# Kernel tuning notes

Hardware: AMD Instinct MI355X
Metric: run time of the kernel (lower is better)

## Reference

```python
import math
import jax, jax.numpy as jnp
import numpy as np

B, T, C = 2, 2048, 2048
H, G = 16, 4          # n_head, n_group
HKV = H // G          # kv heads
HD = C // H           # head dim = 128

def setup_inputs() -> dict:
    key = jax.random.key(0)
    ks = jax.random.split(key, 4)
    s = 0.02  # realistic init scale
    return {
        "x": jax.random.normal(ks[0], (B, T, C), jnp.float32),
        "Wkv": jax.random.normal(ks[1], (C, 2 * C // G), jnp.float32) * s,
        "bkv": jnp.zeros((2 * C // G,), jnp.float32),
        "Wq": jax.random.normal(ks[2], (C, C), jnp.float32) * s,
        "bq": jnp.zeros((C,), jnp.float32),
        "Wp": jax.random.normal(ks[3], (C, C), jnp.float32) * s,
        "bp": jnp.zeros((C,), jnp.float32),
    }

def _expand_kv(t):
    # (B,T,HKV*HD) -> replicate each kv head G times -> (B,H,T,HD)
    t = t.reshape(B, T, HKV, HD)
    t = jnp.broadcast_to(t[:, :, None], (B, T, G, HKV, HD)).reshape(B, T, H, HD)
    return t.transpose(0, 2, 1, 3)

def reference(x, Wkv, bkv, Wq, bq, Wp, bp):
    kv = x @ Wkv + bkv                      # (B,T,2C/G)
    k, v = jnp.split(kv, 2, axis=-1)
    q = (x @ Wq + bq).reshape(B, T, H, HD).transpose(0, 2, 1, 3)  # (B,H,T,HD)
    k = _expand_kv(k)
    v = _expand_kv(v)
    att = jnp.einsum('bhqd,bhkd->bhqk', q, k) * (1.0 / math.sqrt(HD))
    mask = jnp.tril(jnp.ones((T, T), bool))
    att = jnp.where(mask, att, -jnp.inf)
    att = jax.nn.softmax(att, axis=-1)
    y = jnp.einsum('bhqk,bhkd->bhqd', att, v)
    y = y.transpose(0, 2, 1, 3).reshape(B, T, C)
    return y @ Wp + bp
```

## Files before the change

kernel.cpp:

```cpp
#include <hip/hip_runtime.h>

#define Bv 2
#define Tv 2048
#define Cv 2048
#define Hv 16
#define HKVv 4
#define HDv 128

typedef __attribute__((ext_vector_type(8))) __bf16 bf16x8;
typedef __attribute__((ext_vector_type(4))) float floatx4;

__device__ __forceinline__ unsigned short f2b(float f) {
  unsigned int x = __float_as_uint(f);
  x += 0x7fffu + ((x >> 16) & 1u);
  return (unsigned short)(x >> 16);
}

#define MFMA(a, b, c) __builtin_amdgcn_mfma_f32_16x16x32_bf16((a), (b), (c), 0, 0, 0)

__device__ __forceinline__ void gld_lds16(const void* g, void* l) {
  __builtin_amdgcn_global_load_lds((const __attribute__((address_space(1))) void*)g,
                                   (__attribute__((address_space(3))) void*)l, 16, 0, 0);
}

__global__ __launch_bounds__(256) void prep_kernel(
    const float* __restrict__ x, unsigned short* __restrict__ xb,
    const float* __restrict__ Wq, unsigned short* __restrict__ wq_t,
    const float* __restrict__ Wkv, unsigned short* __restrict__ wkv_t,
    const float* __restrict__ Wp, unsigned short* __restrict__ wp_t) {
  __shared__ float tile[32][33];
  int bid = blockIdx.x, tid = threadIdx.x;
  if (bid < 8192) {
    int i = bid * 256 + tid;
    float4 f = ((const float4*)x)[i];
    ushort4 u;
    u.x = f2b(f.x); u.y = f2b(f.y); u.z = f2b(f.z); u.w = f2b(f.w);
    ((ushort4*)xb)[i] = u;
    return;
  }
  const float* src; unsigned short* dst; int N, idx;
  if (bid < 8192 + 4096)      { idx = bid - 8192;  src = Wq;  dst = wq_t;  N = 2048; }
  else if (bid < 8192 + 6144) { idx = bid - 12288; src = Wkv; dst = wkv_t; N = 1024; }
  else                        { idx = bid - 14336; src = Wp;  dst = wp_t;  N = 2048; }
  const int K = 2048;
  int k0 = (idx & 63) * 32, n0 = (idx >> 6) * 32;
  int tx = tid & 31, ty = tid >> 5;
  for (int i = ty; i < 32; i += 8)
    tile[i][tx] = src[(size_t)(k0 + i) * N + n0 + tx];
  __syncthreads();
  for (int i = ty; i < 32; i += 8)
    dst[(size_t)(n0 + i) * K + k0 + tx] = f2b(tile[tx][i]);
}

__global__ __launch_bounds__(256) void gemm_qkv(
    const unsigned short* __restrict__ xb,
    const unsigned short* __restrict__ wq_t,
    const unsigned short* __restrict__ wkv_t,
    const float* __restrict__ bq, const float* __restrict__ bkv,
    unsigned short* __restrict__ qs,
    unsigned short* __restrict__ ks,
    unsigned short* __restrict__ vs) {
  __shared__ __align__(16) unsigned short Ash[2][128 * 32];
  __shared__ __align__(16) unsigned short Bsh[2][128 * 32];
  int tid = threadIdx.x;
  int wave = tid >> 6, lane = tid & 63;
  int c = lane & 15, quad = lane >> 4;
  int wr = (wave >> 1) * 64, wc = (wave & 1) * 64;
  int fid = blockIdx.y * gridDim.x + blockIdx.x;
  int xcd = fid & 7, u = fid >> 3;
  int mr = u & 7, nr = u >> 3;
  int m0 = ((xcd & 3) * 8 + mr) * 128;
  int n0 = ((xcd >> 2) * 12 + nr) * 128;
  bool isq = (n0 < 2048);
  const unsigned short* wt = isq ? (wq_t + (size_t)n0 * 2048)
                                 : (wkv_t + (size_t)(n0 - 2048) * 2048);
  floatx4 zero4 = {0.f, 0.f, 0.f, 0.f};
  floatx4 acc[4][4];
#pragma unroll
  for (int i = 0; i < 4; i++)
#pragma unroll
    for (int j = 0; j < 4; j++) acc[i][j] = zero4;

  const unsigned short* Abase = xb + (size_t)m0 * 2048;
  int s0 = wave * 128 + lane, s1 = wave * 128 + 64 + lane;
  int r0 = s0 >> 2, kc0 = (s0 & 3) ^ ((r0 >> 1) & 3);
  int r1 = s1 >> 2, kc1 = (s1 & 3) ^ ((r1 >> 1) & 3);
  int swz3 = quad ^ ((c >> 1) & 3);
  int dA0 = (wave * 128) * 8, dA1 = (wave * 128 + 64) * 8;

  gld_lds16(Abase + (size_t)r0 * 2048 + kc0 * 8, &Ash[0][0] + dA0);
  gld_lds16(Abase + (size_t)r1 * 2048 + kc1 * 8, &Ash[0][0] + dA1);
  gld_lds16(wt + (size_t)r0 * 2048 + kc0 * 8, &Bsh[0][0] + dA0);
  gld_lds16(wt + (size_t)r1 * 2048 + kc1 * 8, &Bsh[0][0] + dA1);
  __syncthreads();

  for (int it = 0; it < 64; it++) {
    int cur = it & 1;
    if (it + 1 < 64) {
      int k1 = (it + 1) * 32;
      gld_lds16(Abase + (size_t)r0 * 2048 + k1 + kc0 * 8, &Ash[cur ^ 1][0] + dA0);
      gld_lds16(Abase + (size_t)r1 * 2048 + k1 + kc1 * 8, &Ash[cur ^ 1][0] + dA1);
      gld_lds16(wt + (size_t)r0 * 2048 + k1 + kc0 * 8, &Bsh[cur ^ 1][0] + dA0);
      gld_lds16(wt + (size_t)r1 * 2048 + k1 + kc1 * 8, &Bsh[cur ^ 1][0] + dA1);
    }
    bf16x8 af[4], bfv[4];
#pragma unroll
    for (int i = 0; i < 4; i++)
      af[i] = *(const bf16x8*)(&Ash[cur][(wr + i * 16 + c) * 32 + swz3 * 8]);
#pragma unroll
    for (int j = 0; j < 4; j++)
      bfv[j] = *(const bf16x8*)(&Bsh[cur][(wc + j * 16 + c) * 32 + swz3 * 8]);
#pragma unroll
    for (int i = 0; i < 4; i++)
#pragma unroll
      for (int j = 0; j < 4; j++)
        acc[i][j] = MFMA(af[i], bfv[j], acc[i][j]);
    __syncthreads();
  }

#pragma unroll
  for (int i = 0; i < 4; i++) {
#pragma unroll
    for (int j = 0; j < 4; j++) {
#pragma unroll
      for (int r = 0; r < 4; r++) {
        int m = m0 + wr + i * 16 + quad * 4 + r;
        int n = n0 + wc + j * 16 + c;
        int bidx = m >> 11, t = m & 2047;
        float val = acc[i][j][r];
        if (isq) {
          val = (val + bq[n]) * 0.08838834764831845f;
          int hh = n >> 7, d = n & 127;
          qs[((size_t)((bidx * Hv + hh) * Tv) + t) * HDv + d] = f2b(val);
        } else {
          int n2 = n - 2048;
          val += bkv[n2];
          if (n2 < 512) {
            int hh = n2 >> 7, d = n2 & 127;
            ks[((size_t)((bidx * HKVv + hh) * Tv) + t) * HDv + d] = f2b(val);
          } else {
            int n3 = n2 - 512;
            int hh = n3 >> 7, d = n3 & 127;
            vs[((size_t)((bidx * HKVv + hh) * HDv) + d) * Tv + t] = f2b(val);
          }
        }
      }
    }
  }
}

__global__ __launch_bounds__(256, 4) void attn_kernel(
    const unsigned short* __restrict__ qs,
    const unsigned short* __restrict__ ks,
    const unsigned short* __restrict__ vs,
    unsigned short* __restrict__ ys) {
  __shared__ __align__(16) unsigned short Ksh[2][32 * 128];
  __shared__ __align__(16) unsigned short Vsh[2][128 * 32];
  __shared__ __align__(16) unsigned short Psh[4][16 * 32];

  int x = blockIdx.x, h = blockIdx.y, b = blockIdx.z;
  int qt = (h & 8) ? (31 - x) : x;
  int hkv = h & (HKVv - 1);
  int tid = threadIdx.x;
  int wave = tid >> 6, lane = tid & 63;
  int c = lane & 15, quad = lane >> 4;
  int q0w = qt * 64 + wave * 16;
  int qrow = q0w + c;
  int swzK = c & 7, swzV = (c >> 1) & 3;

  const unsigned short* qptr = qs + ((size_t)((b * Hv + h) * Tv) + q0w) * HDv;
  const unsigned short* kbase = ks + (size_t)((b * HKVv + hkv) * Tv) * HDv;
  const unsigned short* vbase = vs + (size_t)((b * HKVv + hkv) * HDv) * Tv;

  bf16x8 qf[4];
#pragma unroll
  for (int kc = 0; kc < 4; kc++)
    qf[kc] = *(const bf16x8*)(qptr + (size_t)c * HDv + kc * 32 + quad * 8);

  floatx4 zero4 = {0.f, 0.f, 0.f, 0.f};
  floatx4 o[8];
#pragma unroll
  for (int dt = 0; dt < 8; dt++) o[dt] = zero4;
  float M = -1e30f, L = 0.f;

  unsigned short* Pw = &Psh[wave][0];

  int kOff[2], vOff[2];
#pragma unroll
  for (int i = 0; i < 2; i++) {
    int s = wave * 128 + i * 64 + lane;
    int rk = s >> 4, gk = (s & 15) ^ (rk & 7);
    kOff[i] = rk * 128 + gk * 8;
    int rv = s >> 2, gv = (s & 3) ^ ((rv >> 1) & 3);
    vOff[i] = rv * Tv + gv * 8;
  }
  int ldsBase = (wave * 128) * 8;

  int ntiles = 2 * qt + 2;

#pragma unroll
  for (int i = 0; i < 2; i++) gld_lds16(kbase + kOff[i], &Ksh[0][0] + ldsBase + i * 512);
#pragma unroll
  for (int i = 0; i < 2; i++) gld_lds16(vbase + vOff[i], &Vsh[0][0] + ldsBase + i * 512);
  __syncthreads();

  for (int kt = 0; kt < ntiles; kt++) {
    int kv0 = kt * 32;
    int cur = kt & 1;
    if (kt + 1 < ntiles) {
      int kv1 = (kt + 1) * 32;
#pragma unroll
      for (int i = 0; i < 2; i++)
        gld_lds16(kbase + (size_t)kv1 * 128 + kOff[i], &Ksh[cur ^ 1][0] + ldsBase + i * 512);
#pragma unroll
      for (int i = 0; i < 2; i++)
        gld_lds16(vbase + kv1 + vOff[i], &Vsh[cur ^ 1][0] + ldsBase + i * 512);
    }

    if (kv0 <= q0w + 15) {
      const unsigned short* Kb = &Ksh[cur][0];
      const unsigned short* Vb = &Vsh[cur][0];
      floatx4 st[2] = {zero4, zero4};
#pragma unroll
      for (int kc = 0; kc < 4; kc++) {
#pragma unroll
        for (int sub = 0; sub < 2; sub++) {
          bf16x8 kf = *(const bf16x8*)(&Kb[(sub * 16 + c) * 128 + (((kc * 4 + quad) ^ swzK) * 8)]);
          st[sub] = MFMA(kf, qf[kc], st[sub]);
        }
      }
      if (kv0 + 31 > q0w) {
#pragma unroll
        for (int sub = 0; sub < 2; sub++) {
          int kvb = kv0 + sub * 16 + quad * 4;
#pragma unroll
          for (int r = 0; r < 4; r++)
            if (kvb + r > qrow) st[sub][r] = -1e30f;
        }
      }
      float mx = -1e30f;
#pragma unroll
      for (int sub = 0; sub < 2; sub++)
        mx = fmaxf(mx, fmaxf(fmaxf(st[sub][0], st[sub][1]), fmaxf(st[sub][2], st[sub][3])));
      mx = fmaxf(mx, __shfl_xor(mx, 16));
      mx = fmaxf(mx, __shfl_xor(mx, 32));
      if (!__all(mx <= M + 8.0f)) {
        float Mn = fmaxf(M, mx);
        float al = __expf(M - Mn);
        M = Mn;
        L *= al;
#pragma unroll
        for (int dt = 0; dt < 8; dt++) o[dt] *= al;
      }
      float l = 0.f;
#pragma unroll
      for (int sub = 0; sub < 2; sub++) {
        float p0 = __expf(st[sub][0] - M);
        float p1 = __expf(st[sub][1] - M);
        float p2 = __expf(st[sub][2] - M);
        float p3 = __expf(st[sub][3] - M);
        l += (p0 + p1) + (p2 + p3);
        unsigned int lo = (unsigned int)f2b(p0) | ((unsigned int)f2b(p1) << 16);
        unsigned int hi = (unsigned int)f2b(p2) | ((unsigned int)f2b(p3) << 16);
        int g = (sub * 2 + (quad >> 1)) ^ swzV;
        *(uint2*)(&Pw[c * 32 + g * 8 + (quad & 1) * 4]) = make_uint2(lo, hi);
      }
      l += __shfl_xor(l, 16);
      l += __shfl_xor(l, 32);
      L += l;
      bf16x8 pf = *(const bf16x8*)(&Pw[c * 32 + ((quad ^ swzV) * 8)]);
#pragma unroll
      for (int dt = 0; dt < 8; dt++) {
        bf16x8 vf = *(const bf16x8*)(&Vb[(dt * 16 + c) * 32 + ((quad ^ swzV) * 8)]);
        o[dt] = MFMA(vf, pf, o[dt]);
      }
    }
    __syncthreads();
  }

  float Li = 1.0f / L;
  size_t rowbase = ((size_t)(b * Tv + qrow)) * Cv + h * HDv;
#pragma unroll
  for (int dt = 0; dt < 8; dt++) {
    unsigned int lo = (unsigned int)f2b(o[dt][0] * Li) | ((unsigned int)f2b(o[dt][1] * Li) << 16);
    unsigned int hi2 = (unsigned int)f2b(o[dt][2] * Li) | ((unsigned int)f2b(o[dt][3] * Li) << 16);
    *(uint2*)(&ys[rowbase + dt * 16 + quad * 4]) = make_uint2(lo, hi2);
  }
}

__global__ __launch_bounds__(256) void gemm_proj(
    const unsigned short* __restrict__ ys,
    const unsigned short* __restrict__ wp_t,
    const float* __restrict__ bp,
    float* __restrict__ out) {
  __shared__ __align__(16) unsigned short Ash[2][128 * 32];
  __shared__ __align__(16) unsigned short Bsh[2][128 * 32];
  int tid = threadIdx.x;
  int wave = tid >> 6, lane = tid & 63;
  int c = lane & 15, quad = lane >> 4;
  int wr = (wave >> 1) * 64, wc = (wave & 1) * 64;
  int fid = blockIdx.y * gridDim.x + blockIdx.x;
  int xcd = fid & 7, u = fid >> 3;
  int mr = u & 7, nr = u >> 3;
  int m0 = ((xcd & 3) * 8 + mr) * 128;
  int n0 = ((xcd >> 2) * 8 + nr) * 128;
  floatx4 zero4 = {0.f, 0.f, 0.f, 0.f};
  floatx4 acc[4][4];
#pragma unroll
  for (int i = 0; i < 4; i++)
#pragma unroll
    for (int j = 0; j < 4; j++) acc[i][j] = zero4;

  const unsigned short* Abase = ys + (size_t)m0 * 2048;
  const unsigned short* Bbase = wp_t + (size_t)n0 * 2048;
  int s0 = wave * 128 + lane, s1 = wave * 128 + 64 + lane;
  int r0 = s0 >> 2, kc0 = (s0 & 3) ^ ((r0 >> 1) & 3);
  int r1 = s1 >> 2, kc1 = (s1 & 3) ^ ((r1 >> 1) & 3);
  int swz3 = quad ^ ((c >> 1) & 3);
  int dA0 = (wave * 128) * 8, dA1 = (wave * 128 + 64) * 8;

  gld_lds16(Abase + (size_t)r0 * 2048 + kc0 * 8, &Ash[0][0] + dA0);
  gld_lds16(Abase + (size_t)r1 * 2048 + kc1 * 8, &Ash[0][0] + dA1);
  gld_lds16(Bbase + (size_t)r0 * 2048 + kc0 * 8, &Bsh[0][0] + dA0);
  gld_lds16(Bbase + (size_t)r1 * 2048 + kc1 * 8, &Bsh[0][0] + dA1);
  __syncthreads();

  for (int it = 0; it < 64; it++) {
    int cur = it & 1;
    if (it + 1 < 64) {
      int k1 = (it + 1) * 32;
      gld_lds16(Abase + (size_t)r0 * 2048 + k1 + kc0 * 8, &Ash[cur ^ 1][0] + dA0);
      gld_lds16(Abase + (size_t)r1 * 2048 + k1 + kc1 * 8, &Ash[cur ^ 1][0] + dA1);
      gld_lds16(Bbase + (size_t)r0 * 2048 + k1 + kc0 * 8, &Bsh[cur ^ 1][0] + dA0);
      gld_lds16(Bbase + (size_t)r1 * 2048 + k1 + kc1 * 8, &Bsh[cur ^ 1][0] + dA1);
    }
    bf16x8 af[4], bfv[4];
#pragma unroll
    for (int i = 0; i < 4; i++)
      af[i] = *(const bf16x8*)(&Ash[cur][(wr + i * 16 + c) * 32 + swz3 * 8]);
#pragma unroll
    for (int j = 0; j < 4; j++)
      bfv[j] = *(const bf16x8*)(&Bsh[cur][(wc + j * 16 + c) * 32 + swz3 * 8]);
#pragma unroll
    for (int i = 0; i < 4; i++)
#pragma unroll
      for (int j = 0; j < 4; j++)
        acc[i][j] = MFMA(af[i], bfv[j], acc[i][j]);
    __syncthreads();
  }

#pragma unroll
  for (int i = 0; i < 4; i++) {
#pragma unroll
    for (int j = 0; j < 4; j++) {
#pragma unroll
      for (int r = 0; r < 4; r++) {
        int m = m0 + wr + i * 16 + quad * 4 + r;
        int n = n0 + wc + j * 16 + c;
        out[(size_t)m * 2048 + n] = acc[i][j][r] + bp[n];
      }
    }
  }
}

extern "C" void kernel_launch(void* const* d_in, const int* in_sizes, int n_in,
                              void* d_out, int out_size, void* d_ws, size_t ws_size,
                              hipStream_t stream) {
  (void)in_sizes; (void)n_in; (void)out_size; (void)ws_size;
  const float* x   = (const float*)d_in[0];
  const float* Wkv = (const float*)d_in[1];
  const float* bkv = (const float*)d_in[2];
  const float* Wq  = (const float*)d_in[3];
  const float* bq  = (const float*)d_in[4];
  const float* Wp  = (const float*)d_in[5];
  const float* bp  = (const float*)d_in[6];
  float* out = (float*)d_out;

  char* ws = (char*)d_ws;
  unsigned short* xb    = (unsigned short*)(ws + 0);
  unsigned short* wq_t  = (unsigned short*)(ws + 16777216);
  unsigned short* wkv_t = (unsigned short*)(ws + 25165824);
  unsigned short* wp_t  = (unsigned short*)(ws + 29360128);
  unsigned short* qs    = (unsigned short*)(ws + 37748736);
  unsigned short* ks    = (unsigned short*)(ws + 54525952);
  unsigned short* vs    = (unsigned short*)(ws + 58720256);
  unsigned short* ysbuf = (unsigned short*)(ws + 62914560);

  prep_kernel<<<18432, 256, 0, stream>>>(x, xb, Wq, wq_t, Wkv, wkv_t, Wp, wp_t);
  gemm_qkv<<<dim3(32, 24), 256, 0, stream>>>(xb, wq_t, wkv_t, bq, bkv, qs, ks, vs);
  attn_kernel<<<dim3(32, 16, 2), 256, 0, stream>>>(qs, ks, vs, ysbuf);
  gemm_proj<<<dim3(32, 16), 256, 0, stream>>>(ysbuf, wp_t, bp, out);
}
```

Measured before the change: 346.2 us.

## Rewrite QKV GEMM as 256x256 tile 8-wave phased pipeline with setprio

The QKV projection GEMM moves from 128x128 tiles with 4 waves and a simple double buffer to 256x256 tiles with 8 waves and a K-step of 64. Global-to-LDS loads are interleaved across four MFMA phases, using explicit vmcnt waits and raw barriers instead of one syncthreads per K step. s_setprio raises wave priority around MFMA bursts, and the attention kernel also gets setprio around its MFMA loops. This is meant to improve data reuse and overlap loads with compute. The cost is 128KB of LDS, a 192-block grid that is under one wave on 256 CUs, and heavy register pressure.

```diff
diff --git a/kernel.cpp b/kernel.cpp
--- a/kernel.cpp
+++ b/kernel.cpp
@@ -52,7 +52,61 @@
     dst[(size_t)(n0 + i) * K + k0 + tx] = f2b(tile[tx][i]);
 }
 
-__global__ __launch_bounds__(256) void gemm_qkv(
+
+#define VMW asm volatile("s_waitcnt vmcnt(4)" ::: "memory")
+
+#define UNIT_A(slot, kt, h)                                                          \
+  {                                                                                  \
+    gld_lds16(Ab + ofsG[(h)*2] + (size_t)(kt) * 64, &Ash[slot][0] + dstL[(h)*2]);    \
+    gld_lds16(Ab + ofsG[(h)*2+1] + (size_t)(kt) * 64, &Ash[slot][0] + dstL[(h)*2+1]);\
+  }
+#define UNIT_B(slot, kt, h)                                                          \
+  {                                                                                  \
+    gld_lds16(wt + ofsG[(h)*2] + (size_t)(kt) * 64, &Bsh[slot][0] + dstL[(h)*2]);    \
+    gld_lds16(wt + ofsG[(h)*2+1] + (size_t)(kt) * 64, &Bsh[slot][0] + dstL[(h)*2+1]);\
+  }
+
+#define PHASE(As, Bs, P, STG, VMC)                                              \
+  {                                                                             \
+    bf16x8 a0k0 = *(const bf16x8*)(&(As)[arow + (2*(P)) * 1024 + ga0]);         \
+    bf16x8 a0k1 = *(const bf16x8*)(&(As)[arow + (2*(P)) * 1024 + ga1]);         \
+    bf16x8 a1k0 = *(const bf16x8*)(&(As)[arow + (2*(P)+1) * 1024 + ga0]);       \
+    bf16x8 a1k1 = *(const bf16x8*)(&(As)[arow + (2*(P)+1) * 1024 + ga1]);       \
+    if ((P) == 0) {                                                             \
+      bq0a = *(const bf16x8*)(&(Bs)[brow + 0 * 1024 + ga0]);                    \
+      bq0b = *(const bf16x8*)(&(Bs)[brow + 0 * 1024 + ga1]);                    \
+      bq1a = *(const bf16x8*)(&(Bs)[brow + 1 * 1024 + ga0]);                    \
+      bq1b = *(const bf16x8*)(&(Bs)[brow + 1 * 1024 + ga1]);                    \
+      bq2a = *(const bf16x8*)(&(Bs)[brow + 2 * 1024 + ga0]);                    \
+      bq2b = *(const bf16x8*)(&(Bs)[brow + 2 * 1024 + ga1]);                    \
+      bq3a = *(const bf16x8*)(&(Bs)[brow + 3 * 1024 + ga0]);                    \
+      bq3b = *(const bf16x8*)(&(Bs)[brow + 3 * 1024 + ga1]);                    \
+    }                                                                           \
+    STG                                                                         \
+    __builtin_amdgcn_s_barrier();                                               \
+    __builtin_amdgcn_s_setprio(1);                                              \
+    acc[2*(P)][0]   = MFMA(a0k0, bq0a, acc[2*(P)][0]);                          \
+    acc[2*(P)][0]   = MFMA(a0k1, bq0b, acc[2*(P)][0]);                          \
+    acc[2*(P)][1]   = MFMA(a0k0, bq1a, acc[2*(P)][1]);                          \
+    acc[2*(P)][1]   = MFMA(a0k1, bq1b, acc[2*(P)][1]);                          \
+    acc[2*(P)][2]   = MFMA(a0k0, bq2a, acc[2*(P)][2]);                          \
+    acc[2*(P)][2]   = MFMA(a0k1, bq2b, acc[2*(P)][2]);                          \
+    acc[2*(P)][3]   = MFMA(a0k0, bq3a, acc[2*(P)][3]);                          \
+    acc[2*(P)][3]   = MFMA(a0k1, bq3b, acc[2*(P)][3]);                          \
+    acc[2*(P)+1][0] = MFMA(a1k0, bq0a, acc[2*(P)+1][0]);                        \
+    acc[2*(P)+1][0] = MFMA(a1k1, bq0b, acc[2*(P)+1][0]);                        \
+    acc[2*(P)+1][1] = MFMA(a1k0, bq1a, acc[2*(P)+1][1]);                        \
+    acc[2*(P)+1][1] = MFMA(a1k1, bq1b, acc[2*(P)+1][1]);                        \
+    acc[2*(P)+1][2] = MFMA(a1k0, bq2a, acc[2*(P)+1][2]);                        \
+    acc[2*(P)+1][2] = MFMA(a1k1, bq2b, acc[2*(P)+1][2]);                        \
+    acc[2*(P)+1][3] = MFMA(a1k0, bq3a, acc[2*(P)+1][3]);                        \
+    acc[2*(P)+1][3] = MFMA(a1k1, bq3b, acc[2*(P)+1][3]);                        \
+    __builtin_amdgcn_s_setprio(0);                                              \
+    VMC;                                                                        \
+    __builtin_amdgcn_s_barrier();                                               \
+  }
+
+__global__ __launch_bounds__(512, 2) void gemm_qkv(
     const unsigned short* __restrict__ xb,
     const unsigned short* __restrict__ wq_t,
     const unsigned short* __restrict__ wkv_t,
@@ -60,88 +114,89 @@
     unsigned short* __restrict__ qs,
     unsigned short* __restrict__ ks,
     unsigned short* __restrict__ vs) {
-  __shared__ __align__(16) unsigned short Ash[2][128 * 32];
-  __shared__ __align__(16) unsigned short Bsh[2][128 * 32];
+  __shared__ __align__(16) unsigned short Ash[2][256 * 64];
+  __shared__ __align__(16) unsigned short Bsh[2][256 * 64];
   int tid = threadIdx.x;
   int wave = tid >> 6, lane = tid & 63;
   int c = lane & 15, quad = lane >> 4;
-  int wr = (wave >> 1) * 64, wc = (wave & 1) * 64;
-  int fid = blockIdx.y * gridDim.x + blockIdx.x;
+  int wm = wave >> 2, wn = wave & 3;
+
+  int fid = blockIdx.x;
   int xcd = fid & 7, u = fid >> 3;
-  int mr = u & 7, nr = u >> 3;
-  int m0 = ((xcd & 3) * 8 + mr) * 128;
-  int n0 = ((xcd >> 2) * 12 + nr) * 128;
+  int mt = (xcd & 3) * 4 + (u & 3);
+  int nt = (xcd >> 2) * 6 + (u >> 2);
+  int m0 = mt * 256, n0 = nt * 256;
   bool isq = (n0 < 2048);
   const unsigned short* wt = isq ? (wq_t + (size_t)n0 * 2048)
                                  : (wkv_t + (size_t)(n0 - 2048) * 2048);
+  const unsigned short* Ab = xb + (size_t)m0 * 2048;
+
   floatx4 zero4 = {0.f, 0.f, 0.f, 0.f};
-  floatx4 acc[4][4];
-#pragma unroll
-  for (int i = 0; i < 4; i++)
+  floatx4 acc[8][4];
+#pragma unroll
+  for (int i = 0; i < 8; i++)
 #pragma unroll
     for (int j = 0; j < 4; j++) acc[i][j] = zero4;
 
-  const unsigned short* Abase = xb + (size_t)m0 * 2048;
-  int s0 = wave * 128 + lane, s1 = wave * 128 + 64 + lane;
-  int r0 = s0 >> 2, kc0 = (s0 & 3) ^ ((r0 >> 1) & 3);
-  int r1 = s1 >> 2, kc1 = (s1 & 3) ^ ((r1 >> 1) & 3);
-  int swz3 = quad ^ ((c >> 1) & 3);
-  int dA0 = (wave * 128) * 8, dA1 = (wave * 128 + 64) * 8;
-
-  gld_lds16(Abase + (size_t)r0 * 2048 + kc0 * 8, &Ash[0][0] + dA0);
-  gld_lds16(Abase + (size_t)r1 * 2048 + kc1 * 8, &Ash[0][0] + dA1);
-  gld_lds16(wt + (size_t)r0 * 2048 + kc0 * 8, &Bsh[0][0] + dA0);
-  gld_lds16(wt + (size_t)r1 * 2048 + kc1 * 8, &Bsh[0][0] + dA1);
-  __syncthreads();
-
-  for (int it = 0; it < 64; it++) {
-    int cur = it & 1;
-    if (it + 1 < 64) {
-      int k1 = (it + 1) * 32;
-      gld_lds16(Abase + (size_t)r0 * 2048 + k1 + kc0 * 8, &Ash[cur ^ 1][0] + dA0);
-      gld_lds16(Abase + (size_t)r1 * 2048 + k1 + kc1 * 8, &Ash[cur ^ 1][0] + dA1);
-      gld_lds16(wt + (size_t)r0 * 2048 + k1 + kc0 * 8, &Bsh[cur ^ 1][0] + dA0);
-      gld_lds16(wt + (size_t)r1 * 2048 + k1 + kc1 * 8, &Bsh[cur ^ 1][0] + dA1);
-    }
-    bf16x8 af[4], bfv[4];
-#pragma unroll
-    for (int i = 0; i < 4; i++)
-      af[i] = *(const bf16x8*)(&Ash[cur][(wr + i * 16 + c) * 32 + swz3 * 8]);
-#pragma unroll
-    for (int j = 0; j < 4; j++)
-      bfv[j] = *(const bf16x8*)(&Bsh[cur][(wc + j * 16 + c) * 32 + swz3 * 8]);
-#pragma unroll
-    for (int i = 0; i < 4; i++)
-#pragma unroll
-      for (int j = 0; j < 4; j++)
-        acc[i][j] = MFMA(af[i], bfv[j], acc[i][j]);
-    __syncthreads();
-  }
-
-#pragma unroll
-  for (int i = 0; i < 4; i++) {
+  int ofsG[4], dstL[4];
+#pragma unroll
+  for (int hl = 0; hl < 4; hl++) {
+    int L = (hl >> 1) * 1024 + (hl & 1) * 512 + tid;
+    int row = L >> 3, g = L & 7;
+    int kg = g ^ (row & 7);
+    ofsG[hl] = row * 2048 + kg * 8;
+    dstL[hl] = L * 8;
+  }
+  int cb = c & 7;
+  int ga0 = (quad ^ cb) * 8;
+  int ga1 = ((4 + quad) ^ cb) * 8;
+  int arow = (wm * 128 + c) * 64;
+  int brow = (wn * 64 + c) * 64;
+
+  bf16x8 bq0a, bq0b, bq1a, bq1b, bq2a, bq2b, bq3a, bq3b;
+
+  UNIT_A(0, 0, 0) UNIT_A(0, 0, 1) UNIT_B(0, 0, 0) UNIT_B(0, 0, 1)
+  UNIT_B(1, 1, 0) UNIT_B(1, 1, 1)
+  VMW;
+  __builtin_amdgcn_s_barrier();
+
+  for (int it2 = 0; it2 < 16; ++it2) {
+    int t = it2 * 2;
+    bool g2 = (t + 2) < 32, g3 = (t + 3) < 32;
+    PHASE(Ash[0], Bsh[0], 0, { UNIT_A(1, t + 1, 0) }, ;)
+    PHASE(Ash[0], Bsh[0], 1, { UNIT_A(1, t + 1, 1) if (g2) UNIT_B(0, t + 2, 0) }, ;)
+    PHASE(Ash[0], Bsh[0], 2, { if (g2) UNIT_B(0, t + 2, 1) }, ;)
+    PHASE(Ash[0], Bsh[0], 3, { }, VMW)
+    PHASE(Ash[1], Bsh[1], 0, { if (g2) UNIT_A(0, t + 2, 0) }, ;)
+    PHASE(Ash[1], Bsh[1], 1, { if (g2) UNIT_A(0, t + 2, 1) if (g3) UNIT_B(1, t + 3, 0) }, ;)
+    PHASE(Ash[1], Bsh[1], 2, { if (g3) UNIT_B(1, t + 3, 1) }, ;)
+    PHASE(Ash[1], Bsh[1], 3, { }, VMW)
+  }
+
+#pragma unroll
+  for (int i = 0; i < 8; i++) {
 #pragma unroll
     for (int j = 0; j < 4; j++) {
 #pragma unroll
       for (int r = 0; r < 4; r++) {
-        int m = m0 + wr + i * 16 + quad * 4 + r;
-        int n = n0 + wc + j * 16 + c;
-        int bidx = m >> 11, t = m & 2047;
+        int m = m0 + wm * 128 + i * 16 + quad * 4 + r;
+        int n = n0 + wn * 64 + j * 16 + c;
+        int bidx = m >> 11, tt = m & 2047;
         float val = acc[i][j][r];
         if (isq) {
           val = (val + bq[n]) * 0.08838834764831845f;
           int hh = n >> 7, d = n & 127;
-          qs[((size_t)((bidx * Hv + hh) * Tv) + t) * HDv + d] = f2b(val);
+          qs[((size_t)((bidx * Hv + hh) * Tv) + tt) * HDv + d] = f2b(val);
         } else {
           int n2 = n - 2048;
           val += bkv[n2];
           if (n2 < 512) {
             int hh = n2 >> 7, d = n2 & 127;
-            ks[((size_t)((bidx * HKVv + hh) * Tv) + t) * HDv + d] = f2b(val);
+            ks[((size_t)((bidx * HKVv + hh) * Tv) + tt) * HDv + d] = f2b(val);
           } else {
             int n3 = n2 - 512;
             int hh = n3 >> 7, d = n3 & 127;
-            vs[((size_t)((bidx * HKVv + hh) * HDv) + d) * Tv + t] = f2b(val);
+            vs[((size_t)((bidx * HKVv + hh) * HDv) + d) * Tv + tt] = f2b(val);
           }
         }
       }
@@ -221,6 +276,7 @@
       const unsigned short* Kb = &Ksh[cur][0];
       const unsigned short* Vb = &Vsh[cur][0];
       floatx4 st[2] = {zero4, zero4};
+      __builtin_amdgcn_s_setprio(1);
 #pragma unroll
       for (int kc = 0; kc < 4; kc++) {
 #pragma unroll
@@ -229,6 +285,7 @@
           st[sub] = MFMA(kf, qf[kc], st[sub]);
         }
       }
+      __builtin_amdgcn_s_setprio(0);
       if (kv0 + 31 > q0w) {
 #pragma unroll
         for (int sub = 0; sub < 2; sub++) {
@@ -269,11 +326,13 @@
       l += __shfl_xor(l, 32);
       L += l;
       bf16x8 pf = *(const bf16x8*)(&Pw[c * 32 + ((quad ^ swzV) * 8)]);
+      __builtin_amdgcn_s_setprio(1);
 #pragma unroll
       for (int dt = 0; dt < 8; dt++) {
         bf16x8 vf = *(const bf16x8*)(&Vb[(dt * 16 + c) * 32 + ((quad ^ swzV) * 8)]);
         o[dt] = MFMA(vf, pf, o[dt]);
       }
+      __builtin_amdgcn_s_setprio(0);
     }
     __syncthreads();
   }
@@ -387,7 +446,7 @@
   unsigned short* ysbuf = (unsigned short*)(ws + 62914560);
 
   prep_kernel<<<18432, 256, 0, stream>>>(x, xb, Wq, wq_t, Wkv, wkv_t, Wp, wp_t);
-  gemm_qkv<<<dim3(32, 24), 256, 0, stream>>>(xb, wq_t, wkv_t, bq, bkv, qs, ks, vs);
+  gemm_qkv<<<192, 512, 0, stream>>>(xb, wq_t, wkv_t, bq, bkv, qs, ks, vs);
   attn_kernel<<<dim3(32, 16, 2), 256, 0, stream>>>(qs, ks, vs, ysbuf);
   gemm_proj<<<dim3(32, 16), 256, 0, stream>>>(ysbuf, wp_t, bp, out);
 }
```

After: 357.0 us. +3.1%, slower.
